# Performance work log

Measured on AMD Instinct MI355X. Metric: run time of the kernel, lower is better.

## Reference

```python
import jax, jax.numpy as jnp
import numpy as np

B, N, C = 8, 4096, 512
NH = 8
HD = C // NH
EPS = 1e-12  # torch F.normalize default eps


def setup_inputs() -> dict:
    key = jax.random.key(0)
    ks = jax.random.split(key, 6)
    x = jax.random.normal(ks[0], (B, N, C), dtype=jnp.float32)
    x_out = jax.random.normal(ks[1], (B, N, C), dtype=jnp.float32)
    # params: torch Linear weight [out,in]; store as [in,out] for x @ W
    W_qkv = jax.random.normal(ks[2], (C, 3 * C), dtype=jnp.float32) * (1.0 / np.sqrt(C))
    temperature = jnp.ones((NH, 1, 1), dtype=jnp.float32)
    W_proj = jax.random.normal(ks[3], (C, C), dtype=jnp.float32) * (1.0 / np.sqrt(C))
    b_proj = jax.random.normal(ks[4], (C,), dtype=jnp.float32) * 0.01
    return {"x": x, "x_out": x_out, "W_qkv": W_qkv, "temperature": temperature,
            "W_proj": W_proj, "b_proj": b_proj, "H": 64, "W": 64}


def _l2norm(t):
    # F.normalize(t, dim=-1): t / max(||t||_2, eps)
    n = jnp.sqrt(jnp.sum(t * t, axis=-1, keepdims=True))
    return t / jnp.maximum(n, EPS)


def reference(x, x_out, W_qkv, temperature, W_proj, b_proj, H, W):
    b, n, c = x.shape
    nh = temperature.shape[0]
    hd = c // nh
    qkv = (x @ W_qkv).reshape(b, n, 3, nh, hd).transpose(2, 0, 3, 1, 4)  # [3,B,nh,N,hd]
    q, k, v = qkv[0], qkv[1], qkv[2]
    # transpose to channel-attention layout [B,nh,hd,N]
    q = jnp.swapaxes(q, -2, -1)
    k = jnp.swapaxes(k, -2, -1)
    v = jnp.swapaxes(v, -2, -1)
    q = _l2norm(q)
    k = _l2norm(k)
    # cross-covariance attention over channels: [B,nh,hd,hd]
    attn = jnp.einsum('bhcn,bhdn->bhcd', q, k) * temperature
    attn = jax.nn.softmax(attn, axis=-1)
    out = jnp.einsum('bhcd,bhdn->bhcn', attn, v)  # [B,nh,hd,N]
    out = out.transpose(0, 3, 1, 2).reshape(b, n, c)
    return out @ W_proj + b_proj
```

## Files before the change

### kernel.cpp

```cpp
#include <hip/hip_runtime.h>
#include <hip/hip_bf16.h>

typedef __attribute__((ext_vector_type(8))) short short8;
typedef __attribute__((ext_vector_type(4))) float f32x4;

#define BQ 8
#define SEQ 4096
#define CH 512
#define NHD 8
#define HD 64
#define K3C 1536
#define MTOK 32768
#define NSPL 8

__device__ __forceinline__ float bfu2f(unsigned int u) {
  u <<= 16;
  float f;
  __builtin_memcpy(&f, &u, 4);
  return f;
}
__device__ __forceinline__ unsigned short f2bfu(float x) {
  __hip_bfloat16 h = __float2bfloat16(x);
  unsigned short u;
  __builtin_memcpy(&u, &h, 2);
  return u;
}

__device__ __forceinline__ void gload_lds16(const void* g, void* l) {
  __builtin_amdgcn_global_load_lds(
      (const __attribute__((address_space(1))) unsigned int*)g,
      (__attribute__((address_space(3))) unsigned int*)l, 16, 0, 0);
}

__global__ __launch_bounds__(256) void cast_f32_bf16(const float* __restrict__ in,
                                                     unsigned short* __restrict__ out, int n4) {
  int stride = gridDim.x * blockDim.x;
  for (int i = blockIdx.x * blockDim.x + threadIdx.x; i < n4; i += stride) {
    float4 v = reinterpret_cast<const float4*>(in)[i];
    ushort4 o;
    o.x = f2bfu(v.x); o.y = f2bfu(v.y); o.z = f2bfu(v.z); o.w = f2bfu(v.w);
    reinterpret_cast<ushort4*>(out)[i] = o;
  }
}

__global__ __launch_bounds__(256) void transpose_cast(const float* __restrict__ in,
                                                      unsigned short* __restrict__ out,
                                                      int R, int Cc) {
  __shared__ float tile[32][33];
  const int tx = threadIdx.x, ty = threadIdx.y;
  const int c0 = blockIdx.x * 32, r0 = blockIdx.y * 32;
  #pragma unroll
  for (int dy = 0; dy < 32; dy += 8)
    tile[ty + dy][tx] = in[(size_t)(r0 + ty + dy) * Cc + (c0 + tx)];
  __syncthreads();
  #pragma unroll
  for (int dy = 0; dy < 32; dy += 8)
    out[(size_t)(c0 + ty + dy) * R + (r0 + tx)] = f2bfu(tile[tx][ty + dy]);
}

template <int MODE>
__global__ __launch_bounds__(512, 2) void gemm256(const unsigned short* __restrict__ A,
                                                  const unsigned short* __restrict__ Bt,
                                                  void* __restrict__ out0,
                                                  void* __restrict__ out1,
                                                  const float* __restrict__ bias,
                                                  int M, int Nn, int Kk, int nbx) {
  __shared__ __align__(16) char lds[131072];
  const int nwg = gridDim.x;
  int wg = blockIdx.x;
  wg = (wg & 7) * (nwg >> 3) + (wg >> 3);
  const int bx = wg % nbx, by = wg / nbx;
  const int m0 = by * 256, n0 = bx * 256;

  const int tid = threadIdx.x, wave = tid >> 6, lane = tid & 63;
  const int wr = wave >> 2, wc = wave & 3;
  const int l15 = lane & 15, lg = lane >> 4;
  const int T = Kk >> 6;

  f32x4 acc[2][4][2][2] = {};
  short8 af[8], b0[4], b1[4];

  auto stageh = [&](int h, int kt, char* buf) {
    const bool isB = (h == 1 || h == 2);
    const unsigned short* src = isB ? Bt : A;
    const int rc0 = isB ? n0 : m0;
    const int rhalf = (h >= 2) ? 128 : 0;
    char* base = buf + (isB ? 32768 : 0);
    #pragma unroll
    for (int j = 0; j < 2; ++j) {
      const int rbase = rhalf + (wave * 2 + j) * 8;
      const unsigned short* g = src + (size_t)(rc0 + rbase + (lane >> 3)) * Kk + kt +
                                (((lane & 7) ^ (lane >> 3)) << 3);
      gload_lds16(g, base + rbase * 128);
    }
  };

  auto dsA = [&](int qa, const char* bufc) {
    #pragma unroll
    for (int fr = 0; fr < 4; ++fr)
      #pragma unroll
      for (int ks = 0; ks < 2; ++ks) {
        const int r = wr * 64 + qa * 128 + fr * 16 + l15;
        const int slot = ((ks << 2) + lg) ^ (r & 7);
        af[fr * 2 + ks] = *reinterpret_cast<const short8*>(bufc + r * 128 + (slot << 4));
      }
  };
  auto dsB = [&](int qb, const char* bufc, short8* bset) {
    #pragma unroll
    for (int fc = 0; fc < 2; ++fc)
      #pragma unroll
      for (int ks = 0; ks < 2; ++ks) {
        const int n = wc * 32 + qb * 128 + fc * 16 + l15;
        const int slot = ((ks << 2) + lg) ^ (n & 7);
        bset[fc * 2 + ks] =
            *reinterpret_cast<const short8*>(bufc + 32768 + n * 128 + (slot << 4));
      }
  };
  auto mfma16 = [&](int qa, int qb, const short8* bset) {
    __builtin_amdgcn_s_setprio(1);
    #pragma unroll
    for (int fr = 0; fr < 4; ++fr)
      #pragma unroll
      for (int fc = 0; fc < 2; ++fc)
        #pragma unroll
        for (int ks = 0; ks < 2; ++ks)
          acc[qa][fr][qb][fc] = __builtin_amdgcn_mfma_f32_16x16x32_bf16(
              af[fr * 2 + ks], bset[fc * 2 + ks], acc[qa][fr][qb][fc], 0, 0, 0);
    __builtin_amdgcn_s_setprio(0);
  };

  stageh(0, 0, lds); stageh(1, 0, lds); stageh(2, 0, lds); stageh(3, 0, lds);
  asm volatile("s_waitcnt vmcnt(0)" ::: "memory");
  __builtin_amdgcn_s_barrier();

  for (int t = 0; t < T - 1; ++t) {
    char* bufc = lds + ((t & 1) << 16);
    char* bufn = lds + (((t + 1) & 1) << 16);
    const int ktn = (t + 1) << 6;

    dsA(0, bufc);
    dsB(0, bufc, b0);
    stageh(0, ktn, bufn);
    stageh(1, ktn, bufn);
    __builtin_amdgcn_sched_barrier(0);
    asm volatile("s_waitcnt vmcnt(6)" ::: "memory");
    __builtin_amdgcn_s_barrier();
    asm volatile("s_waitcnt lgkmcnt(0)" ::: "memory");
    mfma16(0, 0, b0);
    __builtin_amdgcn_s_barrier();

    dsB(1, bufc, b1);
    stageh(2, ktn, bufn);
    __builtin_amdgcn_sched_barrier(0);
    asm volatile("s_waitcnt vmcnt(6)" ::: "memory");
    __builtin_amdgcn_s_barrier();
    asm volatile("s_waitcnt lgkmcnt(0)" ::: "memory");
    mfma16(0, 1, b1);
    __builtin_amdgcn_s_barrier();

    dsA(1, bufc);
    stageh(3, ktn, bufn);
    __builtin_amdgcn_sched_barrier(0);
    asm volatile("s_waitcnt vmcnt(8)" ::: "memory");
    __builtin_amdgcn_s_barrier();
    asm volatile("s_waitcnt lgkmcnt(0)" ::: "memory");
    mfma16(1, 1, b1);
    __builtin_amdgcn_s_barrier();

    asm volatile("s_waitcnt vmcnt(4)" ::: "memory");
    __builtin_amdgcn_s_barrier();
    mfma16(1, 0, b0);
    __builtin_amdgcn_s_barrier();
  }

  asm volatile("s_waitcnt vmcnt(0)" ::: "memory");
  __builtin_amdgcn_s_barrier();
  {
    const char* bufc = lds + (((T - 1) & 1) << 16);
    dsA(0, bufc);
    dsB(0, bufc, b0);
    asm volatile("s_waitcnt lgkmcnt(0)" ::: "memory");
    mfma16(0, 0, b0);
    dsB(1, bufc, b1);
    asm volatile("s_waitcnt lgkmcnt(0)" ::: "memory");
    mfma16(0, 1, b1);
    dsA(1, bufc);
    asm volatile("s_waitcnt lgkmcnt(0)" ::: "memory");
    mfma16(1, 1, b1);
    mfma16(1, 0, b0);
  }

  if (MODE == 1) {
    #pragma unroll
    for (int qa = 0; qa < 2; ++qa)
      #pragma unroll
      for (int fr = 0; fr < 4; ++fr)
        #pragma unroll
        for (int qb = 0; qb < 2; ++qb)
          #pragma unroll
          for (int fc = 0; fc < 2; ++fc) {
            const int row0 = m0 + wr * 64 + qa * 128 + fr * 16 + lg * 4;
            const int col = n0 + wc * 32 + qb * 128 + fc * 16 + l15;
            #pragma unroll
            for (int v = 0; v < 4; ++v)
              reinterpret_cast<float*>(out0)[(size_t)(row0 + v) * Nn + col] =
                  acc[qa][fr][qb][fc][v] + bias[col];
          }
  } else if (n0 < 1024) {
    __builtin_amdgcn_s_barrier();
    char* ldsb = lds;
    #pragma unroll
    for (int qa = 0; qa < 2; ++qa)
      #pragma unroll
      for (int fr = 0; fr < 4; ++fr)
        #pragma unroll
        for (int qb = 0; qb < 2; ++qb)
          #pragma unroll
          for (int fc = 0; fc < 2; ++fc) {
            const int nl = wr * 64 + qa * 128 + fr * 16 + lg * 4;
            const int cl = wc * 32 + qb * 128 + fc * 16 + l15;
            ushort4 o;
            o.x = f2bfu(acc[qa][fr][qb][fc][0]);
            o.y = f2bfu(acc[qa][fr][qb][fc][1]);
            o.z = f2bfu(acc[qa][fr][qb][fc][2]);
            o.w = f2bfu(acc[qa][fr][qb][fc][3]);
            const int byte = cl * 512 + ((nl * 2) ^ ((cl & 7) << 4));
            *reinterpret_cast<ushort4*>(ldsb + byte) = o;
          }
    __builtin_amdgcn_s_barrier();
    #pragma unroll
    for (int it = 0; it < 16; ++it) {
      const int cl = it * 16 + (tid >> 5);
      const int ns = (tid & 31) * 8;
      const int byte = cl * 512 + ((ns * 2) ^ ((cl & 7) << 4));
      short8 val = *reinterpret_cast<const short8*>(ldsb + byte);
      const int gcol = n0 + cl;
      const int sel = gcol >> 9, rem = gcol & 511;
      const int bh = (m0 >> 12) * 8 + (rem >> 6), cc = rem & 63;
      *reinterpret_cast<short8*>(&reinterpret_cast<unsigned short*>(out0)[
          ((size_t)sel * 4096 + bh * 64 + cc) * 4096 + (m0 & 4095) + ns]) = val;
    }
  } else {
    #pragma unroll
    for (int qa = 0; qa < 2; ++qa)
      #pragma unroll
      for (int fr = 0; fr < 4; ++fr)
        #pragma unroll
        for (int qb = 0; qb < 2; ++qb)
          #pragma unroll
          for (int fc = 0; fc < 2; ++fc) {
            const int row0 = m0 + wr * 64 + qa * 128 + fr * 16 + lg * 4;
            const int col = n0 + wc * 32 + qb * 128 + fc * 16 + l15;
            const int rem = col & 511, hh = rem >> 6, cc = rem & 63;
            const int bb = row0 >> 12, nseq = row0 & 4095;
            const int bh = bb * 8 + hh;
            #pragma unroll
            for (int v = 0; v < 4; ++v)
              reinterpret_cast<unsigned short*>(out1)[
                  ((size_t)bh * 4096 + nseq + v) * 64 + cc] =
                  f2bfu(acc[qa][fr][qb][fc][v]);
          }
  }
}

__global__ __launch_bounds__(256) void attn_qk(const unsigned short* __restrict__ qkT,
                                               float* __restrict__ rawp,
                                               float* __restrict__ normp) {
  const int bh = blockIdx.x, s = blockIdx.y;
  const int tid = threadIdx.x, w = tid >> 6, lane = tid & 63;
  const int l15 = lane & 15, lg = lane >> 4;
  const int nbase = s * 512 + w * 128;
  const unsigned short* qrow = qkT + (size_t)(bh * 64) * 4096;
  const unsigned short* krow = qkT + (size_t)(4096 + bh * 64) * 4096;

  __shared__ float red[4][64][64];
  __shared__ float nrm[4][2][64];

  f32x4 acc[4][4] = {};
  float sq[4] = {0.f, 0.f, 0.f, 0.f}, sk[4] = {0.f, 0.f, 0.f, 0.f};

  #pragma unroll
  for (int kc = 0; kc < 2; ++kc) {
    short8 aq[4][2], bk[4][2];
    #pragma unroll
    for (int fr = 0; fr < 4; ++fr)
      #pragma unroll
      for (int ks = 0; ks < 2; ++ks) {
        const size_t off = (size_t)(fr * 16 + l15) * 4096 + nbase + (kc * 2 + ks) * 32 + lg * 8;
        aq[fr][ks] = *reinterpret_cast<const short8*>(&qrow[off]);
        bk[fr][ks] = *reinterpret_cast<const short8*>(&krow[off]);
      }
    #pragma unroll
    for (int ks = 0; ks < 2; ++ks)
      #pragma unroll
      for (int fr = 0; fr < 4; ++fr)
        #pragma unroll
        for (int fc = 0; fc < 4; ++fc)
          acc[fr][fc] = __builtin_amdgcn_mfma_f32_16x16x32_bf16(
              aq[fr][ks], bk[fc][ks], acc[fr][fc], 0, 0, 0);
    #pragma unroll
    for (int fr = 0; fr < 4; ++fr)
      #pragma unroll
      for (int ks = 0; ks < 2; ++ks)
        #pragma unroll
        for (int j = 0; j < 8; ++j) {
          const float fq = bfu2f((unsigned short)aq[fr][ks][j]);
          const float fk = bfu2f((unsigned short)bk[fr][ks][j]);
          sq[fr] = fmaf(fq, fq, sq[fr]);
          sk[fr] = fmaf(fk, fk, sk[fr]);
        }
  }

  #pragma unroll
  for (int fr = 0; fr < 4; ++fr) {
    sq[fr] += __shfl_xor(sq[fr], 16); sq[fr] += __shfl_xor(sq[fr], 32);
    sk[fr] += __shfl_xor(sk[fr], 16); sk[fr] += __shfl_xor(sk[fr], 32);
  }
  if (lane < 16) {
    #pragma unroll
    for (int fr = 0; fr < 4; ++fr) {
      nrm[w][0][fr * 16 + lane] = sq[fr];
      nrm[w][1][fr * 16 + lane] = sk[fr];
    }
  }
  #pragma unroll
  for (int fr = 0; fr < 4; ++fr)
    #pragma unroll
    for (int fc = 0; fc < 4; ++fc)
      #pragma unroll
      for (int v = 0; v < 4; ++v)
        red[w][fr * 16 + lg * 4 + v][fc * 16 + l15] = acc[fr][fc][v];
  __syncthreads();

  const float* rf = &red[0][0][0];
  float* rp = rawp + ((size_t)s * 64 + bh) * 4096;
  for (int i = tid; i < 4096; i += 256)
    rp[i] = rf[i] + rf[4096 + i] + rf[8192 + i] + rf[12288 + i];
  const float* nf = &nrm[0][0][0];
  if (tid < 128) {
    float* np = normp + ((size_t)s * 64 + bh) * 128;
    np[tid] = nf[tid] + nf[128 + tid] + nf[256 + tid] + nf[384 + tid];
  }
}

__global__ __launch_bounds__(64) void attn_finalize(const float* __restrict__ rawp,
                                                    const float* __restrict__ normp,
                                                    const float* __restrict__ temperature,
                                                    unsigned short* __restrict__ attnP) {
  const int bh = blockIdx.x, c8 = blockIdx.y, h = bh & 7;
  const int d = threadIdx.x;
  float nq = 0.f, nk = 0.f;
  for (int s = 0; s < NSPL; ++s) {
    nq += normp[((size_t)s * 64 + bh) * 128 + d];
    nk += normp[((size_t)s * 64 + bh) * 128 + 64 + d];
  }
  nq = fmaxf(sqrtf(nq), 1e-12f);
  nk = fmaxf(sqrtf(nk), 1e-12f);
  const float t = temperature[h];
  for (int i = 0; i < 8; ++i) {
    const int c = c8 * 8 + i;
    float r = 0.f;
    for (int s = 0; s < NSPL; ++s)
      r += rawp[((size_t)s * 64 + bh) * 4096 + c * 64 + d];
    const float nqc = __shfl(nq, c);
    float v = r * t / (nqc * nk);
    float m = v;
    #pragma unroll
    for (int off = 32; off > 0; off >>= 1) m = fmaxf(m, __shfl_xor(m, off));
    float e = __expf(v - m);
    float ssum = e;
    #pragma unroll
    for (int off = 32; off > 0; off >>= 1) ssum += __shfl_xor(ssum, off);
    attnP[(size_t)bh * 4096 + c * 64 + d] = f2bfu(e / ssum);
  }
}

__global__ __launch_bounds__(256) void pv_mfma(const unsigned short* __restrict__ attnP,
                                               const unsigned short* __restrict__ vb,
                                               unsigned short* __restrict__ y) {
  const int nc = blockIdx.x, bh = blockIdx.y;
  const int b = bh >> 3, h = bh & 7;
  const int tid = threadIdx.x, w = tid >> 6, lane = tid & 63;
  const int l15 = lane & 15, lg = lane >> 4;
  const int n0 = nc * 256 + w * 64;

  short8 ap[4][2], bv[4][2];
  #pragma unroll
  for (int fr = 0; fr < 4; ++fr)
    #pragma unroll
    for (int ks = 0; ks < 2; ++ks)
      ap[fr][ks] = *reinterpret_cast<const short8*>(
          &attnP[(size_t)bh * 4096 + (fr * 16 + l15) * 64 + ks * 32 + lg * 8]);
  #pragma unroll
  for (int fc = 0; fc < 4; ++fc)
    #pragma unroll
    for (int ks = 0; ks < 2; ++ks)
      bv[fc][ks] = *reinterpret_cast<const short8*>(
          &vb[((size_t)bh * 4096 + n0 + fc * 16 + l15) * 64 + ks * 32 + lg * 8]);

  f32x4 acc[4][4] = {};
  #pragma unroll
  for (int ks = 0; ks < 2; ++ks)
    #pragma unroll
    for (int fr = 0; fr < 4; ++fr)
      #pragma unroll
      for (int fc = 0; fc < 4; ++fc)
        acc[fr][fc] = __builtin_amdgcn_mfma_f32_16x16x32_bf16(
            ap[fr][ks], bv[fc][ks], acc[fr][fc], 0, 0, 0);

  #pragma unroll
  for (int fr = 0; fr < 4; ++fr)
    #pragma unroll
    for (int fc = 0; fc < 4; ++fc) {
      const int n = n0 + fc * 16 + l15;
      const int c0 = fr * 16 + lg * 4;
      ushort4 o;
      o.x = f2bfu(acc[fr][fc][0]); o.y = f2bfu(acc[fr][fc][1]);
      o.z = f2bfu(acc[fr][fc][2]); o.w = f2bfu(acc[fr][fc][3]);
      *reinterpret_cast<ushort4*>(
          &y[((size_t)b * 4096 + n) * 512 + h * 64 + c0]) = o;
    }
}

extern "C" void kernel_launch(void* const* d_in, const int* in_sizes, int n_in,
                              void* d_out, int out_size, void* d_ws, size_t ws_size,
                              hipStream_t stream) {
  const float* x = (const float*)d_in[0];
  const float* Wqkv = (const float*)d_in[2];
  const float* temp = (const float*)d_in[3];
  const float* Wproj = (const float*)d_in[4];
  const float* bproj = (const float*)d_in[5];
  float* out = (float*)d_out;

  char* w = (char*)d_ws;
  unsigned short* xb = (unsigned short*)w;    w += (size_t)MTOK * CH * 2;
  unsigned short* wqT = (unsigned short*)w;   w += (size_t)K3C * CH * 2;
  unsigned short* wpT = (unsigned short*)w;   w += (size_t)CH * CH * 2;
  unsigned short* qkT = (unsigned short*)w;   w += (size_t)2 * 64 * 64 * 4096 * 2;
  unsigned short* vb = (unsigned short*)w;    w += (size_t)64 * 4096 * 64 * 2;
  unsigned short* yb = (unsigned short*)w;    w += (size_t)MTOK * CH * 2;
  float* rawp = (float*)w;                    w += (size_t)NSPL * 64 * 4096 * 4;
  float* normp = (float*)w;                   w += (size_t)NSPL * 64 * 128 * 4;
  unsigned short* attnP = (unsigned short*)w; w += (size_t)64 * 4096 * 2;

  cast_f32_bf16<<<2048, 256, 0, stream>>>(x, xb, MTOK * CH / 4);
  transpose_cast<<<dim3(K3C / 32, CH / 32), dim3(32, 8), 0, stream>>>(Wqkv, wqT, CH, K3C);
  transpose_cast<<<dim3(CH / 32, CH / 32), dim3(32, 8), 0, stream>>>(Wproj, wpT, CH, CH);
  gemm256<0><<<768, 512, 0, stream>>>(xb, wqT, qkT, vb, nullptr, MTOK, K3C, CH, 6);
  attn_qk<<<dim3(64, 8), 256, 0, stream>>>(qkT, rawp, normp);
  attn_finalize<<<dim3(64, 8), 64, 0, stream>>>(rawp, normp, temp, attnP);
  pv_mfma<<<dim3(16, 64), 256, 0, stream>>>(attnP, vb, yb);
  gemm256<1><<<256, 512, 0, stream>>>(yb, wpT, out, nullptr, bproj, MTOK, CH, CH, 2);
}
```

Baseline: 157.6 us.

## Simplify GEMM main loop to one barrier per K-tile with bulk prefetch

Folds the peeled final K-iteration back into the main loop, using a predicate to skip prefetching on the last tile. Instead of interleaving four partial global-to-LDS stage loads with per-quadrant vmcnt waits and barrier pairs, it issues all four next-tile stage loads up front. It then runs the four MFMA quadrants and does a single vmcnt(0) wait plus one barrier per iteration. This cuts barrier and wait overhead and drops the explicit lgkmcnt waits and sched_barriers, leaving instruction ordering to the compiler. The trade-off is less fine-grained overlap between memory traffic and MFMA work, and it relies on the compiler to place waits correctly for the LDS reads.

```diff
diff --git a/kernel.cpp b/kernel.cpp
--- a/kernel.cpp
+++ b/kernel.cpp
@@ -133,61 +133,26 @@
   asm volatile("s_waitcnt vmcnt(0)" ::: "memory");
   __builtin_amdgcn_s_barrier();
 
-  for (int t = 0; t < T - 1; ++t) {
+  for (int t = 0; t < T; ++t) {
     char* bufc = lds + ((t & 1) << 16);
     char* bufn = lds + (((t + 1) & 1) << 16);
     const int ktn = (t + 1) << 6;
+    const bool st = (t < T - 1);
 
     dsA(0, bufc);
     dsB(0, bufc, b0);
-    stageh(0, ktn, bufn);
-    stageh(1, ktn, bufn);
-    __builtin_amdgcn_sched_barrier(0);
-    asm volatile("s_waitcnt vmcnt(6)" ::: "memory");
-    __builtin_amdgcn_s_barrier();
-    asm volatile("s_waitcnt lgkmcnt(0)" ::: "memory");
-    mfma16(0, 0, b0);
-    __builtin_amdgcn_s_barrier();
-
-    dsB(1, bufc, b1);
-    stageh(2, ktn, bufn);
-    __builtin_amdgcn_sched_barrier(0);
-    asm volatile("s_waitcnt vmcnt(6)" ::: "memory");
-    __builtin_amdgcn_s_barrier();
-    asm volatile("s_waitcnt lgkmcnt(0)" ::: "memory");
-    mfma16(0, 1, b1);
-    __builtin_amdgcn_s_barrier();
-
-    dsA(1, bufc);
-    stageh(3, ktn, bufn);
-    __builtin_amdgcn_sched_barrier(0);
-    asm volatile("s_waitcnt vmcnt(8)" ::: "memory");
-    __builtin_amdgcn_s_barrier();
-    asm volatile("s_waitcnt lgkmcnt(0)" ::: "memory");
-    mfma16(1, 1, b1);
-    __builtin_amdgcn_s_barrier();
-
-    asm volatile("s_waitcnt vmcnt(4)" ::: "memory");
-    __builtin_amdgcn_s_barrier();
-    mfma16(1, 0, b0);
-    __builtin_amdgcn_s_barrier();
-  }
-
-  asm volatile("s_waitcnt vmcnt(0)" ::: "memory");
-  __builtin_amdgcn_s_barrier();
-  {
-    const char* bufc = lds + (((T - 1) & 1) << 16);
-    dsA(0, bufc);
-    dsB(0, bufc, b0);
-    asm volatile("s_waitcnt lgkmcnt(0)" ::: "memory");
+    if (st) {
+      stageh(0, ktn, bufn); stageh(1, ktn, bufn);
+      stageh(2, ktn, bufn); stageh(3, ktn, bufn);
+    }
     mfma16(0, 0, b0);
     dsB(1, bufc, b1);
-    asm volatile("s_waitcnt lgkmcnt(0)" ::: "memory");
     mfma16(0, 1, b1);
     dsA(1, bufc);
-    asm volatile("s_waitcnt lgkmcnt(0)" ::: "memory");
     mfma16(1, 1, b1);
     mfma16(1, 0, b0);
+    if (st) asm volatile("s_waitcnt vmcnt(0)" ::: "memory");
+    __builtin_amdgcn_s_barrier();
   }
 
   if (MODE == 1) {
@@ -207,7 +172,6 @@
                   acc[qa][fr][qb][fc][v] + bias[col];
           }
   } else if (n0 < 1024) {
-    __builtin_amdgcn_s_barrier();
     char* ldsb = lds;
     #pragma unroll
     for (int qa = 0; qa < 2; ++qa)
```

Measured after the change: 158.7 us. No clear change (+0.7%).
